# Optimization experiments

Hardware: AMD Instinct MI355X
Metric: run time of the kernel (lower is better)

## Reference

```python
import jax, jax.numpy as jnp
import numpy as np

C_IN, C_P1, C_G1, N_OUT = 512, 256, 256, 6
B, H, W = 256, 19, 19


def mish(x):
    return x * jnp.tanh(jax.nn.softplus(x))


def setup_inputs() -> dict:
    key = jax.random.key(0)
    ks = jax.random.split(key, 8)
    x = jax.random.normal(ks[0], (B, C_IN, H, W), dtype=jnp.float32)
    mask = jnp.ones((B, 1, H, W), dtype=jnp.float32)
    conv1p_w = jax.random.normal(ks[1], (C_P1, C_IN), dtype=jnp.float32) * (1.0 / np.sqrt(C_IN))
    conv1g_w = jax.random.normal(ks[2], (C_G1, C_IN), dtype=jnp.float32) * (1.0 / np.sqrt(C_IN))
    beta_g = jnp.zeros((C_G1,), dtype=jnp.float32)
    linear_g_w = jax.random.normal(ks[3], (C_P1, 3 * C_G1), dtype=jnp.float32) * (1.0 / np.sqrt(3 * C_G1))
    beta2 = jnp.zeros((C_P1,), dtype=jnp.float32)
    conv2p_w = jax.random.normal(ks[4], (N_OUT, C_P1), dtype=jnp.float32) * (0.3 / np.sqrt(C_P1))
    return {"x": x, "mask": mask, "conv1p_w": conv1p_w, "conv1g_w": conv1g_w,
            "beta_g": beta_g, "linear_g_w": linear_g_w, "beta2": beta2, "conv2p_w": conv2p_w}


def reference(x, mask, conv1p_w, conv1g_w, beta_g, linear_g_w, beta2, conv2p_w):
    # 1x1 convs are channel GEMMs
    outp = jnp.einsum('bchw,oc->bohw', x, conv1p_w)              # [B, C_P1, H, W]
    outg = jnp.einsum('bchw,oc->bohw', x, conv1g_w)              # [B, C_G1, H, W]
    # BiasMask (scale=None) + Mish
    outg = mish((outg + beta_g[None, :, None, None]) * mask)
    # KataGPool: mean, scaled mean, max (masked)
    mask_sum_hw = jnp.sum(mask, axis=(2, 3), keepdims=True)      # [B,1,1,1]
    layer_mean = jnp.sum(outg * mask, axis=(2, 3), keepdims=True) / mask_sum_hw
    layer_max = jnp.max(outg + (mask - 1.0), axis=(2, 3), keepdims=True)
    sqrt_off = (jnp.sqrt(mask_sum_hw) - 14.0) / 10.0
    pooled = jnp.concatenate([layer_mean, layer_mean * sqrt_off, layer_max], axis=1)  # [B, 3*C_G1, 1, 1]
    pooled = pooled[:, :, 0, 0]                                  # [B, 3*C_G1]
    g = pooled @ linear_g_w.T                                    # [B, C_P1]
    # broadcast-add, BiasMask, Mish
    outp = mish((outp + g[:, :, None, None] + beta2[None, :, None, None]) * mask)
    # final 1x1 conv + invalid-move penalty
    outp = jnp.einsum('bchw,oc->bohw', outp, conv2p_w)           # [B, 6, H, W]
    outp = outp - (1.0 - mask) * 5000.0
    return outp.reshape(outp.shape[0], outp.shape[1], -1)        # [B, 6, H*W]
```

## Files before the change

### kernel.cpp

```cpp
#include <hip/hip_runtime.h>
#include <math.h>

#define BATCH 256
#define CIN   512
#define CP    256
#define HW    361
#define NOUT  6
#define NT    6

typedef short bf16x8 __attribute__((ext_vector_type(8)));
typedef short bf16x4 __attribute__((ext_vector_type(4)));
typedef float f32x4  __attribute__((ext_vector_type(4)));

__device__ __forceinline__ short f2bf(float f) {
    unsigned u = __float_as_uint(f);
    u += 0x7fffu + ((u >> 16) & 1u);
    return (short)(u >> 16);
}
__device__ __forceinline__ float bf2f(short s) {
    return __uint_as_float(((unsigned)(unsigned short)s) << 16);
}
__device__ __forceinline__ float mish_f(float v) {
    float u = __expf(v);
    float a = 1.f + u;
    float w = a * a;
    float r = v * (w - 1.f) * __builtin_amdgcn_rcpf(w + 1.f);
    return (v > 30.f) ? v : r;
}
__device__ __forceinline__ void gl_lds16(const void* g, void* l) {
    __builtin_amdgcn_global_load_lds(
        (const __attribute__((address_space(1))) void*)g,
        (__attribute__((address_space(3))) void*)l, 16, 0, 0);
}

__global__ __launch_bounds__(256) void k0_weights(
    const float* __restrict__ w1p, const float* __restrict__ w1g,
    short* __restrict__ wT)
{
    int g = blockIdx.x * 256 + threadIdx.x;
    int kb  = g >> 11;
    int row = (g >> 2) & 511;
    int s   = g & 3;
    int sc  = s ^ ((row >> 1) & 3);
    const float* src = (row < 256) ? (w1p + (size_t)row * CIN)
                                   : (w1g + (size_t)(row - 256) * CIN);
    int c = kb * 32 + sc * 8;
    float f[8];
    *(float4*)(f)     = *(const float4*)(src + c);
    *(float4*)(f + 4) = *(const float4*)(src + c + 4);
    bf16x8 v;
    #pragma unroll
    for (int i = 0; i < 8; ++i) v[i] = f2bf(f[i]);
    *(bf16x8*)((char*)wT + (size_t)kb * 32768 + row * 64 + s * 16) = v;
}

__global__ __launch_bounds__(512, 4) void k1_conv1(
    const float* __restrict__ x, const short* __restrict__ wT,
    const float* __restrict__ mask, const float* __restrict__ beta_g,
    short* __restrict__ outp_pre, float* __restrict__ psum, float* __restrict__ pmax)
{
    int orig = blockIdx.x;
    int newid = (orig & 7) * 192 + (orig >> 3);
    int n = newid % NT;
    int b = newid / NT;

    const int tid = threadIdx.x;
    const int lane = tid & 63, wid = tid >> 6;
    const int lc = lane & 15, lg = lane >> 4;
    const int hw0 = n * 64;

    __shared__ __align__(16) short As[2][16384];
    __shared__ __align__(16) short Bs[2][2048];
    __shared__ float maskS[64];
    __shared__ float betaS[256];

    if (tid < 64) {
        int hwg_ = hw0 + tid;
        maskS[tid] = (hwg_ < HW) ? mask[b * HW + hwg_] : 0.f;
    }
    if (tid < 256) betaS[tid] = beta_g[tid];
    asm volatile("s_waitcnt vmcnt(0) lgkmcnt(0)" ::: "memory");
    __builtin_amdgcn_sched_barrier(0);

    const int brow = tid & 63;
    const int q    = tid >> 6;
    const int hwg  = hw0 + brow;
    const bool bvalid = hwg < HW;
    const float* xq = x + ((size_t)b * CIN + q * 4) * HW + hwg;
    const int bDstOff = brow * 64 + (((q >> 1) ^ ((brow >> 1) & 3)) * 16) + ((q & 1) * 8);
    char* bDstBase = (char*)Bs;

    const char* aSrc = (const char*)wT + tid * 16;
    char* aDst = (char*)As + tid * 16;

    int aOff[4], bOff[4];
    #pragma unroll
    for (int mf = 0; mf < 4; ++mf) {
        int r = wid * 64 + mf * 16 + lc;
        aOff[mf] = r * 64 + ((lg ^ ((r >> 1) & 3)) * 16);
    }
    #pragma unroll
    for (int nf = 0; nf < 4; ++nf) {
        int r = nf * 16 + lc;
        bOff[nf] = r * 64 + ((lg ^ ((r >> 1) & 3)) * 16);
    }

    float regB[2][4];
    #pragma unroll
    for (int i = 0; i < 4; ++i) { regB[0][i] = 0.f; regB[1][i] = 0.f; }

    f32x4 acc[4][4];
    #pragma unroll
    for (int i = 0; i < 4; ++i)
        #pragma unroll
        for (int j = 0; j < 4; ++j)
            acc[i][j] = (f32x4){0.f, 0.f, 0.f, 0.f};

#define BLOAD(SET, kb)                                                     \
    do {                                                                   \
        const float* src_ = xq + (size_t)(kb) * 32 * HW;                   \
        _Pragma("unroll")                                                  \
        for (int i_ = 0; i_ < 4; ++i_)                                     \
            regB[SET][i_] = bvalid ? src_[(size_t)i_ * HW] : 0.f;          \
    } while (0)

#define BWRITE(SET, buf)                                                   \
    do {                                                                   \
        bf16x4 o_;                                                         \
        _Pragma("unroll")                                                  \
        for (int i_ = 0; i_ < 4; ++i_) o_[i_] = f2bf(regB[SET][i_]);       \
        *(bf16x4*)(bDstBase + (buf) * 4096 + bDstOff) = o_;                \
    } while (0)

#define ALOAD(buf, kb)                                                     \
    do {                                                                   \
        _Pragma("unroll")                                                  \
        for (int l_ = 0; l_ < 4; ++l_)                                     \
            gl_lds16(aSrc + (size_t)(kb) * 32768 + l_ * 8192,              \
                     aDst + (buf) * 32768 + l_ * 8192);                    \
    } while (0)

    BLOAD(0, 0);
    ALOAD(0, 0);
    asm volatile("s_waitcnt vmcnt(4)" ::: "memory");
    __builtin_amdgcn_sched_barrier(0);
    BWRITE(0, 0);
    BLOAD(1, 1);
    asm volatile("s_waitcnt vmcnt(4)" ::: "memory");
    __builtin_amdgcn_sched_barrier(0);
    asm volatile("s_waitcnt lgkmcnt(0)" ::: "memory");
    __builtin_amdgcn_s_barrier();
    __builtin_amdgcn_sched_barrier(0);

    #pragma unroll
    for (int t = 0; t < 16; ++t) {
        const char* ab = (const char*)As + (t & 1) * 32768;
        const char* bb = (const char*)Bs + (t & 1) * 4096;

        bf16x8 aF[4], bF[4];
        #pragma unroll
        for (int mf = 0; mf < 4; ++mf) aF[mf] = *(const bf16x8*)(ab + aOff[mf]);
        #pragma unroll
        for (int nf = 0; nf < 4; ++nf) bF[nf] = *(const bf16x8*)(bb + bOff[nf]);

        if (t < 15) ALOAD((t + 1) & 1, t + 1);
        if (t < 14) BLOAD(t & 1, t + 2);

        __builtin_amdgcn_s_setprio(1);
        #pragma unroll
        for (int mf = 0; mf < 4; ++mf)
            #pragma unroll
            for (int nf = 0; nf < 4; ++nf)
                acc[mf][nf] = __builtin_amdgcn_mfma_f32_16x16x32_bf16(
                    aF[mf], bF[nf], acc[mf][nf], 0, 0, 0);
        __builtin_amdgcn_s_setprio(0);

        if (t < 15) {
            if (t < 14) {
                asm volatile("s_waitcnt vmcnt(4)" ::: "memory");
            } else {
                asm volatile("s_waitcnt vmcnt(0)" ::: "memory");
            }
            __builtin_amdgcn_sched_barrier(0);
            BWRITE((t + 1) & 1, (t + 1) & 1);
            asm volatile("s_waitcnt lgkmcnt(0)" ::: "memory");
            __builtin_amdgcn_s_barrier();
            __builtin_amdgcn_sched_barrier(0);
        }
    }

    if (wid < 4) {
        #pragma unroll
        for (int mf = 0; mf < 4; ++mf) {
            int ch = wid * 64 + mf * 16 + lg * 4;
            #pragma unroll
            for (int nf = 0; nf < 4; ++nf) {
                int hw = hw0 + nf * 16 + lc;
                if (hw < HW) {
                    #pragma unroll
                    for (int j = 0; j < 4; ++j)
                        outp_pre[((size_t)(b * CP + ch + j)) * HW + hw] = f2bf(acc[mf][nf][j]);
                }
            }
        }
    } else {
        #pragma unroll
        for (int mf = 0; mf < 4; ++mf) {
            #pragma unroll
            for (int j = 0; j < 4; ++j) {
                int rloc = (wid - 4) * 64 + mf * 16 + lg * 4 + j;
                float beta = betaS[rloc];
                float s = 0.f, mx = -INFINITY;
                #pragma unroll
                for (int nf = 0; nf < 4; ++nf) {
                    int cl = nf * 16 + lc;
                    int hw = hw0 + cl;
                    float mv = maskS[cl];
                    float val = mish_f((acc[mf][nf][j] + beta) * mv);
                    if (hw < HW) {
                        s += val * mv;
                        mx = fmaxf(mx, val + mv - 1.f);
                    }
                }
                #pragma unroll
                for (int off = 1; off < 16; off <<= 1) {
                    s += __shfl_xor(s, off, 64);
                    mx = fmaxf(mx, __shfl_xor(mx, off, 64));
                }
                if (lc == 0) {
                    psum[((size_t)(b * CP + rloc)) * NT + n] = s;
                    pmax[((size_t)(b * CP + rloc)) * NT + n] = mx;
                }
            }
        }
    }
#undef BLOAD
#undef BWRITE
#undef ALOAD
}

__global__ __launch_bounds__(256) void k2_pool_linear(
    const float* __restrict__ mask, const float* __restrict__ psum,
    const float* __restrict__ pmax, const float* __restrict__ lw,
    float* __restrict__ g_out)
{
    int b = blockIdx.x, t = threadIdx.x;
    __shared__ float pooled[768];
    __shared__ float msr[4];

    float s = 0.f;
    for (int i = t; i < HW; i += 256) s += mask[b * HW + i];
    #pragma unroll
    for (int off = 1; off < 64; off <<= 1) s += __shfl_xor(s, off, 64);
    if ((t & 63) == 0) msr[t >> 6] = s;
    __syncthreads();
    float msum = msr[0] + msr[1] + msr[2] + msr[3];

    {
        int c = t;
        const float* ps = psum + (size_t)(b * CP + c) * NT;
        const float* pm = pmax + (size_t)(b * CP + c) * NT;
        float s3 = 0.f, m3 = -INFINITY;
        #pragma unroll
        for (int i = 0; i < NT; ++i) { s3 += ps[i]; m3 = fmaxf(m3, pm[i]); }
        float mean = s3 / msum;
        float sq = (sqrtf(msum) - 14.f) * 0.1f;
        pooled[c] = mean; pooled[256 + c] = mean * sq; pooled[512 + c] = m3;
    }
    __syncthreads();
    {
        int o = t;
        const float4* wrow = (const float4*)(lw + (size_t)o * 768);
        float acc = 0.f;
        #pragma unroll 8
        for (int j = 0; j < 192; ++j) {
            float4 w4 = wrow[j];
            float4 p4 = *(const float4*)&pooled[j * 4];
            acc += p4.x * w4.x + p4.y * w4.y + p4.z * w4.z + p4.w * w4.w;
        }
        g_out[b * CP + o] = acc;
    }
}

__global__ __launch_bounds__(256) void k3_final(
    const short* __restrict__ outp_pre, const float* __restrict__ mask,
    const float* __restrict__ g_out, const float* __restrict__ beta2,
    const float* __restrict__ w2, float* __restrict__ out)
{
    int ht = blockIdx.x, b = blockIdx.y;
    int t = threadIdx.x;
    __shared__ float w2S[NOUT * 256];
    __shared__ float gbS[256];
    __shared__ float part[NOUT][256];

    for (int i = t; i < NOUT * 256; i += 256) w2S[i] = w2[i];
    gbS[t] = g_out[b * CP + t] + beta2[t];
    __syncthreads();

    int hw = t & 63, cg = t >> 6;
    int hwg = ht * 64 + hw;
    bool valid = hwg < HW;
    float maskv = valid ? mask[b * HW + hwg] : 0.f;

    float acc[NOUT] = {0.f, 0.f, 0.f, 0.f, 0.f, 0.f};
    const short* src = outp_pre + ((size_t)(b * CP + cg * 64)) * HW + hwg;
    #pragma unroll 4
    for (int ci = 0; ci < 64; ++ci) {
        float v = valid ? bf2f(src[(size_t)ci * HW]) : 0.f;
        float mm = mish_f((v + gbS[cg * 64 + ci]) * maskv);
        #pragma unroll
        for (int o = 0; o < NOUT; ++o) acc[o] += mm * w2S[o * 256 + cg * 64 + ci];
    }
    #pragma unroll
    for (int o = 0; o < NOUT; ++o) part[o][t] = acc[o];
    __syncthreads();

    for (int idx = t; idx < NOUT * 64; idx += 256) {
        int o = idx >> 6, h2 = idx & 63;
        int hg = ht * 64 + h2;
        if (hg < HW) {
            float mv = mask[b * HW + hg];
            float sum = part[o][h2] + part[o][64 + h2] + part[o][128 + h2] + part[o][192 + h2];
            out[((size_t)(b * NOUT + o)) * HW + hg] = sum - (1.f - mv) * 5000.f;
        }
    }
}

extern "C" void kernel_launch(void* const* d_in, const int* in_sizes, int n_in,
                              void* d_out, int out_size, void* d_ws, size_t ws_size,
                              hipStream_t stream) {
    const float* x     = (const float*)d_in[0];
    const float* mask  = (const float*)d_in[1];
    const float* w1p   = (const float*)d_in[2];
    const float* w1g   = (const float*)d_in[3];
    const float* betag = (const float*)d_in[4];
    const float* lw    = (const float*)d_in[5];
    const float* beta2 = (const float*)d_in[6];
    const float* w2    = (const float*)d_in[7];
    float* out = (float*)d_out;

    char* ws = (char*)d_ws;
    short* outp_pre = (short*)(ws);
    short* wT       = (short*)(ws + 47316992);
    float* psum     = (float*)(ws + 47841280);
    float* pmax     = (float*)(ws + 49414144);
    float* g_out    = (float*)(ws + 50987008);

    hipLaunchKernelGGL(k0_weights, dim3(128), dim3(256), 0, stream, w1p, w1g, wT);
    hipLaunchKernelGGL(k1_conv1, dim3(1536), dim3(512), 0, stream,
                       x, wT, mask, betag, outp_pre, psum, pmax);
    hipLaunchKernelGGL(k2_pool_linear, dim3(BATCH), dim3(256), 0, stream,
                       mask, psum, pmax, lw, g_out);
    hipLaunchKernelGGL(k3_final, dim3(6, BATCH), dim3(256), 0, stream,
                       outp_pre, mask, g_out, beta2, w2, out);
    (void)in_sizes; (void)n_in; (void)out_size; (void)ws_size;
}
```

Before: 141.7 us.

## Load conv1 weight fragments directly into registers instead of staging through LDS

The weight (A) operand of the conv1 GEMM is now read straight from global memory into double-buffered registers, replacing the global-to-LDS async copies and the LDS fragment reads. The weight pre-pack kernel drops its XOR swizzle and writes a plain row-major fragment layout that matches the direct register loads. This frees 64 KB of LDS per block and cuts LDS traffic. In exchange it adds register pressure and leaves the weight loads to ordinary global and cache latency, with the explicit vmcnt waits removed and ordering left to the compiler.

Measured after the change: 168.3 us. 18.8% more time.

```diff
diff --git a/kernel.cpp b/kernel.cpp
--- a/kernel.cpp
+++ b/kernel.cpp
@@ -26,11 +26,6 @@
     float w = a * a;
     float r = v * (w - 1.f) * __builtin_amdgcn_rcpf(w + 1.f);
     return (v > 30.f) ? v : r;
-}
-__device__ __forceinline__ void gl_lds16(const void* g, void* l) {
-    __builtin_amdgcn_global_load_lds(
-        (const __attribute__((address_space(1))) void*)g,
-        (__attribute__((address_space(3))) void*)l, 16, 0, 0);
 }
 
 __global__ __launch_bounds__(256) void k0_weights(
@@ -40,18 +35,17 @@
     int g = blockIdx.x * 256 + threadIdx.x;
     int kb  = g >> 11;
     int row = (g >> 2) & 511;
-    int s   = g & 3;
-    int sc  = s ^ ((row >> 1) & 3);
+    int lg  = g & 3;
     const float* src = (row < 256) ? (w1p + (size_t)row * CIN)
                                    : (w1g + (size_t)(row - 256) * CIN);
-    int c = kb * 32 + sc * 8;
+    int c = kb * 32 + lg * 8;
     float f[8];
     *(float4*)(f)     = *(const float4*)(src + c);
     *(float4*)(f + 4) = *(const float4*)(src + c + 4);
     bf16x8 v;
     #pragma unroll
     for (int i = 0; i < 8; ++i) v[i] = f2bf(f[i]);
-    *(bf16x8*)((char*)wT + (size_t)kb * 32768 + row * 64 + s * 16) = v;
+    *(bf16x8*)((char*)wT + (((size_t)kb * 512 + row) * 4 + lg) * 16) = v;
 }
 
 __global__ __launch_bounds__(512, 4) void k1_conv1(
@@ -69,7 +63,6 @@
     const int lc = lane & 15, lg = lane >> 4;
     const int hw0 = n * 64;
 
-    __shared__ __align__(16) short As[2][16384];
     __shared__ __align__(16) short Bs[2][2048];
     __shared__ float maskS[64];
     __shared__ float betaS[256];
@@ -79,8 +72,6 @@
         maskS[tid] = (hwg_ < HW) ? mask[b * HW + hwg_] : 0.f;
     }
     if (tid < 256) betaS[tid] = beta_g[tid];
-    asm volatile("s_waitcnt vmcnt(0) lgkmcnt(0)" ::: "memory");
-    __builtin_amdgcn_sched_barrier(0);
 
     const int brow = tid & 63;
     const int q    = tid >> 6;
@@ -90,15 +81,9 @@
     const int bDstOff = brow * 64 + (((q >> 1) ^ ((brow >> 1) & 3)) * 16) + ((q & 1) * 8);
     char* bDstBase = (char*)Bs;
 
-    const char* aSrc = (const char*)wT + tid * 16;
-    char* aDst = (char*)As + tid * 16;
-
-    int aOff[4], bOff[4];
-    #pragma unroll
-    for (int mf = 0; mf < 4; ++mf) {
-        int r = wid * 64 + mf * 16 + lc;
-        aOff[mf] = r * 64 + ((lg ^ ((r >> 1) & 3)) * 16);
-    }
+    const char* aBase = (const char*)wT + ((size_t)(wid * 64 + lc) * 4 + lg) * 16;
+
+    int bOff[4];
     #pragma unroll
     for (int nf = 0; nf < 4; ++nf) {
         int r = nf * 16 + lc;
@@ -109,6 +94,7 @@
     #pragma unroll
     for (int i = 0; i < 4; ++i) { regB[0][i] = 0.f; regB[1][i] = 0.f; }
 
+    bf16x8 aR[2][4];
     f32x4 acc[4][4];
     #pragma unroll
     for (int i = 0; i < 4; ++i)
@@ -132,39 +118,32 @@
         *(bf16x4*)(bDstBase + (buf) * 4096 + bDstOff) = o_;                \
     } while (0)
 
-#define ALOAD(buf, kb)                                                     \
+#define ALOADR(SET, kb)                                                    \
     do {                                                                   \
         _Pragma("unroll")                                                  \
-        for (int l_ = 0; l_ < 4; ++l_)                                     \
-            gl_lds16(aSrc + (size_t)(kb) * 32768 + l_ * 8192,              \
-                     aDst + (buf) * 32768 + l_ * 8192);                    \
+        for (int mf_ = 0; mf_ < 4; ++mf_)                                  \
+            aR[SET][mf_] = *(const bf16x8*)(aBase +                        \
+                ((size_t)(kb) * 512 + mf_ * 16) * 64);                     \
     } while (0)
 
+    ALOADR(0, 0);
     BLOAD(0, 0);
-    ALOAD(0, 0);
-    asm volatile("s_waitcnt vmcnt(4)" ::: "memory");
-    __builtin_amdgcn_sched_barrier(0);
     BWRITE(0, 0);
     BLOAD(1, 1);
-    asm volatile("s_waitcnt vmcnt(4)" ::: "memory");
-    __builtin_amdgcn_sched_barrier(0);
-    asm volatile("s_waitcnt lgkmcnt(0)" ::: "memory");
-    __builtin_amdgcn_s_barrier();
-    __builtin_amdgcn_sched_barrier(0);
+    __syncthreads();
 
     #pragma unroll
     for (int t = 0; t < 16; ++t) {
-        const char* ab = (const char*)As + (t & 1) * 32768;
-        const char* bb = (const char*)Bs + (t & 1) * 4096;
-
-        bf16x8 aF[4], bF[4];
-        #pragma unroll
-        for (int mf = 0; mf < 4; ++mf) aF[mf] = *(const bf16x8*)(ab + aOff[mf]);
-        #pragma unroll
-        for (int nf = 0; nf < 4; ++nf) bF[nf] = *(const bf16x8*)(bb + bOff[nf]);
-
-        if (t < 15) ALOAD((t + 1) & 1, t + 1);
-        if (t < 14) BLOAD(t & 1, t + 2);
+        const int p  = t & 1;
+        const int np = p ^ 1;
+
+        if (t < 15) ALOADR(np, t + 1);
+        if (t < 14) BLOAD(p, t + 2);
+
+        bf16x8 bF[4];
+        #pragma unroll
+        for (int nf = 0; nf < 4; ++nf)
+            bF[nf] = *(const bf16x8*)((const char*)Bs + p * 4096 + bOff[nf]);
 
         __builtin_amdgcn_s_setprio(1);
         #pragma unroll
@@ -172,18 +151,13 @@
             #pragma unroll
             for (int nf = 0; nf < 4; ++nf)
                 acc[mf][nf] = __builtin_amdgcn_mfma_f32_16x16x32_bf16(
-                    aF[mf], bF[nf], acc[mf][nf], 0, 0, 0);
+                    aR[p][mf], bF[nf], acc[mf][nf], 0, 0, 0);
         __builtin_amdgcn_s_setprio(0);
 
         if (t < 15) {
-            if (t < 14) {
-                asm volatile("s_waitcnt vmcnt(4)" ::: "memory");
-            } else {
-                asm volatile("s_waitcnt vmcnt(0)" ::: "memory");
-            }
+            BWRITE(np, np);
+            asm volatile("s_waitcnt lgkmcnt(0)" ::: "memory");
             __builtin_amdgcn_sched_barrier(0);
-            BWRITE((t + 1) & 1, (t + 1) & 1);
-            asm volatile("s_waitcnt lgkmcnt(0)" ::: "memory");
             __builtin_amdgcn_s_barrier();
             __builtin_amdgcn_sched_barrier(0);
         }
@@ -236,7 +210,7 @@
     }
 #undef BLOAD
 #undef BWRITE
-#undef ALOAD
+#undef ALOADR
 }
 
 __global__ __launch_bounds__(256) void k2_pool_linear(
```
